# Kernel optimization log

Measured on AMD Instinct MI355X. Metric: run time of the kernel, lower is better.

Reference implementation:

```python
import jax, jax.numpy as jnp
import numpy as np


def setup_inputs() -> dict:
    key = jax.random.key(0)
    k1, k2, k3, k4 = jax.random.split(key, 4)
    N, E, d_i, d_o = 4096, 32768, 128, 128
    x = jax.random.normal(k1, (N, d_i), dtype=jnp.float32)
    src = jax.random.uniform(k2, (N, E), dtype=jnp.float32)
    tgt = jax.random.uniform(k3, (N, E), dtype=jnp.float32)
    # Linear(2*d_i, d_o): weight [d_o, 2*d_i] (xavier-like scale), bias zeros
    f_w = jax.random.normal(k4, (d_o, 2 * d_i), dtype=jnp.float32) * (1.0 / np.sqrt(2 * d_i))
    f_b = jnp.zeros((d_o,), dtype=jnp.float32)
    return {"x": x, "src": src, "tgt": tgt, "f_w": f_w, "f_b": f_b}


def reference(x, src, tgt, f_w, f_b):
    # gather node features to edges via dense incidence matmuls
    hsrc = src.T @ x                      # [E, d_i]
    htgt = tgt.T @ x                      # [E, d_i]
    h = jnp.concatenate([hsrc, htgt], axis=1)  # [E, 2*d_i]
    y = jax.nn.relu(h @ f_w.T + f_b)      # [E, d_o]
    return tgt @ y                        # scatter back to nodes: [N, d_o]
```

## Files before the change

kernel.cpp:

```cpp
#include <hip/hip_runtime.h>

typedef __attribute__((ext_vector_type(8))) short short8v;
typedef __attribute__((ext_vector_type(4))) float float4v;
typedef __attribute__((ext_vector_type(2))) unsigned int u32x2;
typedef __attribute__((ext_vector_type(4))) unsigned int u32x4;
typedef unsigned short u16;
typedef unsigned int u32;
typedef const __attribute__((address_space(1))) void* gas1;
typedef __attribute__((address_space(3))) void* las3;

#define NN 4096
#define EE 32768
#define DI 128
#define DO 128

__device__ __forceinline__ u16 f2bf(float f) {
    u32 u = __builtin_bit_cast(u32, f);
    u32 r = u + 0x7fffu + ((u >> 16) & 1u);
    return (u16)(r >> 16);
}
__device__ __forceinline__ u32 pack2bf(float lo, float hi) {
    return (u32)f2bf(lo) | ((u32)f2bf(hi) << 16);
}
__device__ __forceinline__ void gload16(const void* g, void* l) {
    __builtin_amdgcn_global_load_lds((gas1)g, (las3)l, 16, 0, 0);
}
__device__ __forceinline__ u32 cvtpk(float lo, float hi) {
    u32 r;
    asm("v_cvt_pk_bf16_f32 %0, %1, %2" : "=v"(r) : "v"(lo), "v"(hi));
    return r;
}

template<int R, int C>
__device__ __forceinline__ void stage_f32_bf16(char* lds, const float* src, int ld) {
    constexpr int CH = C / 8;
    constexpr int ITER = (R * CH) / 256;
#pragma unroll
    for (int it = 0; it < ITER; ++it) {
        int c = it * 256 + (int)threadIdx.x;
        int row = c / CH, col8 = c % CH;
        const float* p = src + (size_t)row * ld + col8 * 8;
        float4v v0 = *(const float4v*)p;
        float4v v1 = *(const float4v*)(p + 4);
        u32x4 w;
        w[0] = pack2bf(v0[0], v0[1]);
        w[1] = pack2bf(v0[2], v0[3]);
        w[2] = pack2bf(v1[0], v1[1]);
        w[3] = pack2bf(v1[2], v1[3]);
        int kb = col8 * 16;
        *(u32x4*)(lds + row * (C * 2) + (kb ^ ((row & 7) << 4))) = w;
    }
}
template<int ROWB>
__device__ __forceinline__ short8v ldfrag(const char* base, int row16, int kk) {
    int l = (int)threadIdx.x & 63;
    int row = row16 + (l & 15);
    int kb = kk * 64 + ((l >> 4) << 4);
    return *(const short8v*)(base + row * ROWB + (kb ^ ((row & 7) << 4)));
}

__global__ __launch_bounds__(256) void k1_ab(const float* __restrict__ x,
                                             const float* __restrict__ fw,
                                             u16* __restrict__ ATB) {
    __shared__ __align__(16) char lds[64 * 1024];
    char* aL = lds;
    char* bL = lds + 32 * 1024;
    int mb = (int)blockIdx.x >> 5, nb = (int)blockIdx.x & 31;
    stage_f32_bf16<128, 128>(aL, fw + mb * 128, 2 * DI);
    stage_f32_bf16<128, 128>(bL, x + (size_t)nb * 128 * DI, DI);
    __syncthreads();
    int w = (int)threadIdx.x >> 6, l = (int)threadIdx.x & 63;
    int wr = w >> 1, wc = w & 1;
    float4v acc[4][4] = {};
#pragma unroll
    for (int kk = 0; kk < 4; ++kk) {
        short8v af[4], bf[4];
#pragma unroll
        for (int m = 0; m < 4; ++m) af[m] = ldfrag<256>(aL, wr * 64 + m * 16, kk);
#pragma unroll
        for (int n2 = 0; n2 < 4; ++n2) bf[n2] = ldfrag<256>(bL, wc * 64 + n2 * 16, kk);
#pragma unroll
        for (int m = 0; m < 4; ++m)
#pragma unroll
            for (int n2 = 0; n2 < 4; ++n2)
                acc[m][n2] = __builtin_amdgcn_mfma_f32_16x16x32_bf16(af[m], bf[n2], acc[m][n2], 0, 0, 0);
    }
#pragma unroll
    for (int m = 0; m < 4; ++m)
#pragma unroll
        for (int n2 = 0; n2 < 4; ++n2)
#pragma unroll
            for (int r = 0; r < 4; ++r) {
                int mo = mb * 128 + wr * 64 + m * 16 + ((l >> 4) << 2) + r;
                int n  = nb * 128 + wc * 64 + n2 * 16 + (l & 15);
                ATB[(size_t)mo * NN + n] = f2bf(acc[m][n2][r]);
            }
}

__global__ __launch_bounds__(256, 2) void k2_y(const float* __restrict__ src,
                                               const float* __restrict__ tgt,
                                               const u16* __restrict__ ATB,
                                               const float* __restrict__ fb,
                                               u16* __restrict__ YT) {
    __shared__ __align__(16) char lds[48 * 1024];
    const int eb = (int)blockIdx.x * 64;
    const int t = (int)threadIdx.x, w = t >> 6, l = t & 63;
    const int eq = t & 15, nq = t >> 4;

    float4v r0, r1, r2, r3;
    auto loadT = [&](int ks) {
        const float* M = (ks >= 64 ? tgt : src);
        const int n0 = (ks & 63) * 64;
        const float* p = M + (size_t)(n0 + nq * 4) * EE + eb + eq * 4;
        r0 = *(const float4v*)p;
        r1 = *(const float4v*)(p + EE);
        r2 = *(const float4v*)(p + 2 * EE);
        r3 = *(const float4v*)(p + 3 * EE);
    };
    auto gloadA = [&](int ks, int p) {
        const int mat = ks >> 6, n0 = (ks & 63) * 64;
        const u16* AB = ATB + (size_t)mat * 128 * NN + n0;
#pragma unroll
        for (int q = 0; q < 4; ++q) {
            const int s = w * 4 + q;
            const int r = s * 8 + (l >> 3);
            const u16* ga = AB + (size_t)r * NN + (((l & 7) ^ (r & 7)) << 3);
            gload16(ga, lds + p * 16384 + s * 1024);
        }
    };
    auto writeT = [&](int p) {
        char* buf = lds + 32768 + p * 8192;
#pragma unroll
        for (int j = 0; j < 4; ++j) {
            int e = eq * 4 + j;
            u32x2 w2;
            w2[0] = cvtpk(r0[j], r1[j]);
            w2[1] = cvtpk(r2[j], r3[j]);
            *(u32x2*)(buf + e * 128 + ((nq * 8) ^ ((e & 7) << 4))) = w2;
        }
    };

    loadT(0);
    gloadA(0, 0);
    writeT(0);
    __syncthreads();

    float4v acc[2][4] = {};
    for (int ks = 0; ks < 128; ++ks) {
        const int nx = ks < 127 ? ks + 1 : 127;
        loadT(nx);
        gloadA(nx, (ks + 1) & 1);
        asm volatile("s_waitcnt vmcnt(8)" ::: "memory");
        __builtin_amdgcn_sched_barrier(0);
        const char* bufA = lds + (ks & 1) * 16384;
        const char* bufB = lds + 32768 + (ks & 1) * 8192;
        short8v af[2][2], bfr[2][4];
#pragma unroll
        for (int kk = 0; kk < 2; ++kk) {
#pragma unroll
            for (int m = 0; m < 2; ++m)
                af[kk][m] = ldfrag<128>(bufA, w * 32 + m * 16, kk);
#pragma unroll
            for (int n2 = 0; n2 < 4; ++n2)
                bfr[kk][n2] = ldfrag<128>(bufB, n2 * 16, kk);
        }
#pragma unroll
        for (int kk = 0; kk < 2; ++kk)
#pragma unroll
            for (int m = 0; m < 2; ++m)
#pragma unroll
                for (int n2 = 0; n2 < 4; ++n2)
                    acc[m][n2] = __builtin_amdgcn_mfma_f32_16x16x32_bf16(
                        af[kk][m], bfr[kk][n2], acc[m][n2], 0, 0, 0);
        asm volatile("s_waitcnt vmcnt(4)" ::: "memory");
        __builtin_amdgcn_sched_barrier(0);
        writeT((ks + 1) & 1);
        asm volatile("s_waitcnt lgkmcnt(0)" ::: "memory");
        __builtin_amdgcn_sched_barrier(0);
        __builtin_amdgcn_s_barrier();
    }
#pragma unroll
    for (int m = 0; m < 2; ++m)
#pragma unroll
        for (int n2 = 0; n2 < 4; ++n2)
#pragma unroll
            for (int r = 0; r < 4; ++r) {
                const int o = w * 32 + m * 16 + ((l >> 4) << 2) + r;
                const int e = eb + n2 * 16 + (l & 15);
                float v = acc[m][n2][r] + fb[o];
                v = v > 0.f ? v : 0.f;
                YT[(size_t)o * EE + e] = f2bf(v);
            }
}

__global__ __launch_bounds__(256, 2) void k3_part(const float* __restrict__ tgt,
                                                  const u16* __restrict__ YT,
                                                  float* __restrict__ part) {
    __shared__ __align__(16) char lds[64 * 1024];
    const int bid = (int)blockIdx.x;
    const int mb = bid & 63, kc = bid >> 6;
    const int e0 = kc * 2048;
    const int t = (int)threadIdx.x, w = t >> 6, l = t & 63;
    const int wr = w >> 1, wc = w & 1;

    auto stage = [&](int es, int p) {
        const int ec = e0 + es * 64;
#pragma unroll
        for (int q = 0; q < 4; ++q) {
            const int s = w * 4 + q;
            {
                const int r = s * 4 + (l >> 4);
                const float* gp = tgt + (size_t)(mb * 64 + r) * EE + ec
                                  + (((l & 15) ^ (r & 7)) << 2);
                gload16(gp, lds + p * 16384 + s * 1024);
            }
            {
                const int r = s * 8 + (l >> 3);
                const u16* gy = YT + (size_t)r * EE + ec + (((l & 7) ^ (r & 7)) << 3);
                gload16(gy, lds + 32768 + p * 16384 + s * 1024);
            }
        }
    };

    stage(0, 0);
    float4v acc[2][4] = {};
    for (int es = 0; es < 32; ++es) {
        stage(es < 31 ? es + 1 : 31, (es + 1) & 1);
        asm volatile("s_waitcnt vmcnt(8)" ::: "memory");
        __builtin_amdgcn_sched_barrier(0);
        __builtin_amdgcn_s_barrier();
        const char* bufT = lds + (es & 1) * 16384;
        const char* bufY = lds + 32768 + (es & 1) * 16384;
#pragma unroll
        for (int kk = 0; kk < 2; ++kk) {
            short8v af[2];
#pragma unroll
            for (int m = 0; m < 2; ++m) {
                const int row = wr * 32 + m * 16 + (l & 15);
                const int c0 = kk * 8 + ((l >> 4) << 1);
                float4v v0 = *(const float4v*)(bufT + row * 256 + ((c0 ^ (row & 7)) << 4));
                float4v v1 = *(const float4v*)(bufT + row * 256 + (((c0 + 1) ^ (row & 7)) << 4));
                u32x4 aw;
                aw[0] = cvtpk(v0[0], v0[1]);
                aw[1] = cvtpk(v0[2], v0[3]);
                aw[2] = cvtpk(v1[0], v1[1]);
                aw[3] = cvtpk(v1[2], v1[3]);
                af[m] = __builtin_bit_cast(short8v, aw);
            }
#pragma unroll
            for (int n2 = 0; n2 < 4; ++n2) {
                const int row = wc * 64 + n2 * 16 + (l & 15);
                short8v bf = *(const short8v*)(bufY + row * 128 +
                             ((kk * 64 + ((l >> 4) << 4)) ^ ((row & 7) << 4)));
#pragma unroll
                for (int m = 0; m < 2; ++m)
                    acc[m][n2] = __builtin_amdgcn_mfma_f32_16x16x32_bf16(
                        af[m], bf, acc[m][n2], 0, 0, 0);
            }
        }
        __builtin_amdgcn_sched_barrier(0);
        __builtin_amdgcn_s_barrier();
    }
#pragma unroll
    for (int m = 0; m < 2; ++m)
#pragma unroll
        for (int n2 = 0; n2 < 4; ++n2)
#pragma unroll
            for (int r = 0; r < 4; ++r) {
                const int n = mb * 64 + wr * 32 + m * 16 + ((l >> 4) << 2) + r;
                const int o = wc * 64 + n2 * 16 + (l & 15);
                part[((size_t)kc * NN + n) * DO + o] = acc[m][n2][r];
            }
}

__global__ __launch_bounds__(256) void k4_red(const float* __restrict__ part,
                                              float* __restrict__ out) {
    size_t i = ((size_t)blockIdx.x * 256 + threadIdx.x) * 4;
    float4v s = {0.f, 0.f, 0.f, 0.f};
#pragma unroll
    for (int kc = 0; kc < 16; ++kc)
        s += *(const float4v*)(part + (size_t)kc * NN * DO + i);
    *(float4v*)(out + i) = s;
}

extern "C" void kernel_launch(void* const* d_in, const int* in_sizes, int n_in,
                              void* d_out, int out_size, void* d_ws, size_t ws_size,
                              hipStream_t stream) {
    const float* x   = (const float*)d_in[0];
    const float* src = (const float*)d_in[1];
    const float* tgt = (const float*)d_in[2];
    const float* fw  = (const float*)d_in[3];
    const float* fb  = (const float*)d_in[4];
    float* out = (float*)d_out;

    char* ws = (char*)d_ws;
    u16*   ATB  = (u16*)ws;
    u16*   YT   = (u16*)(ws + (size_t)2 * 1024 * 1024);
    float* PART = (float*)(ws + (size_t)16 * 1024 * 1024);

    k1_ab  <<<64,   256, 0, stream>>>(x, fw, ATB);
    k2_y   <<<512,  256, 0, stream>>>(src, tgt, ATB, fb, YT);
    k3_part<<<1024, 256, 0, stream>>>(tgt, YT, PART);
    k4_red <<<512,  256, 0, stream>>>(PART, out);
}
```

Before: 320.1 us.

## Halve k2 edge tile for more blocks; stage tgt as bf16 in k3 LDS

k2_y now handles 32 edges per block instead of 64 and launches 1024 blocks. It uses less LDS and fewer accumulators, and its launch bound targets 4 blocks per SM, so the tgt/src streaming spreads across more CUs. k3_part now loads tgt through registers and converts it to bf16 once before writing to LDS. This replaces the old path that staged fp32 and converted during every fragment read, shrinking LDS so 3 blocks fit per SM. The trade-off is less data reuse per k2 block, since the ATB tile is now reloaded for every 32 edges, plus extra register-staged loads in k3.

```diff
diff --git a/kernel.cpp b/kernel.cpp
--- a/kernel.cpp
+++ b/kernel.cpp
@@ -97,25 +97,23 @@
             }
 }
 
-__global__ __launch_bounds__(256, 2) void k2_y(const float* __restrict__ src,
+__global__ __launch_bounds__(256, 4) void k2_y(const float* __restrict__ src,
                                                const float* __restrict__ tgt,
                                                const u16* __restrict__ ATB,
                                                const float* __restrict__ fb,
                                                u16* __restrict__ YT) {
-    __shared__ __align__(16) char lds[48 * 1024];
-    const int eb = (int)blockIdx.x * 64;
+    __shared__ __align__(16) char lds[40 * 1024];
+    const int eb = (int)blockIdx.x * 32;
     const int t = (int)threadIdx.x, w = t >> 6, l = t & 63;
-    const int eq = t & 15, nq = t >> 4;
-
-    float4v r0, r1, r2, r3;
+    const int eq = t & 7, np = t >> 3;
+
+    float4v r0, r1;
     auto loadT = [&](int ks) {
         const float* M = (ks >= 64 ? tgt : src);
         const int n0 = (ks & 63) * 64;
-        const float* p = M + (size_t)(n0 + nq * 4) * EE + eb + eq * 4;
+        const float* p = M + (size_t)(n0 + 2 * np) * EE + eb + eq * 4;
         r0 = *(const float4v*)p;
         r1 = *(const float4v*)(p + EE);
-        r2 = *(const float4v*)(p + 2 * EE);
-        r3 = *(const float4v*)(p + 3 * EE);
     };
     auto gloadA = [&](int ks, int p) {
         const int mat = ks >> 6, n0 = (ks & 63) * 64;
@@ -129,14 +127,11 @@
         }
     };
     auto writeT = [&](int p) {
-        char* buf = lds + 32768 + p * 8192;
+        char* buf = lds + 32768 + p * 4096;
 #pragma unroll
         for (int j = 0; j < 4; ++j) {
             int e = eq * 4 + j;
-            u32x2 w2;
-            w2[0] = cvtpk(r0[j], r1[j]);
-            w2[1] = cvtpk(r2[j], r3[j]);
-            *(u32x2*)(buf + e * 128 + ((nq * 8) ^ ((e & 7) << 4))) = w2;
+            *(u32*)(buf + e * 128 + ((np * 4) ^ ((e & 7) << 4))) = cvtpk(r0[j], r1[j]);
         }
     };
 
@@ -145,23 +140,23 @@
     writeT(0);
     __syncthreads();
 
-    float4v acc[2][4] = {};
+    float4v acc[2][2] = {};
     for (int ks = 0; ks < 128; ++ks) {
         const int nx = ks < 127 ? ks + 1 : 127;
         loadT(nx);
         gloadA(nx, (ks + 1) & 1);
-        asm volatile("s_waitcnt vmcnt(8)" ::: "memory");
+        asm volatile("s_waitcnt vmcnt(6)" ::: "memory");
         __builtin_amdgcn_sched_barrier(0);
         const char* bufA = lds + (ks & 1) * 16384;
-        const char* bufB = lds + 32768 + (ks & 1) * 8192;
-        short8v af[2][2], bfr[2][4];
+        const char* bufB = lds + 32768 + (ks & 1) * 4096;
+        short8v af[2][2], bfr[2][2];
 #pragma unroll
         for (int kk = 0; kk < 2; ++kk) {
 #pragma unroll
             for (int m = 0; m < 2; ++m)
                 af[kk][m] = ldfrag<128>(bufA, w * 32 + m * 16, kk);
 #pragma unroll
-            for (int n2 = 0; n2 < 4; ++n2)
+            for (int n2 = 0; n2 < 2; ++n2)
                 bfr[kk][n2] = ldfrag<128>(bufB, n2 * 16, kk);
         }
 #pragma unroll
@@ -169,7 +164,7 @@
 #pragma unroll
             for (int m = 0; m < 2; ++m)
 #pragma unroll
-                for (int n2 = 0; n2 < 4; ++n2)
+                for (int n2 = 0; n2 < 2; ++n2)
                     acc[m][n2] = __builtin_amdgcn_mfma_f32_16x16x32_bf16(
                         af[kk][m], bfr[kk][n2], acc[m][n2], 0, 0, 0);
         asm volatile("s_waitcnt vmcnt(4)" ::: "memory");
@@ -182,7 +177,7 @@
 #pragma unroll
     for (int m = 0; m < 2; ++m)
 #pragma unroll
-        for (int n2 = 0; n2 < 4; ++n2)
+        for (int n2 = 0; n2 < 2; ++n2)
 #pragma unroll
             for (int r = 0; r < 4; ++r) {
                 const int o = w * 32 + m * 16 + ((l >> 4) << 2) + r;
@@ -193,71 +188,83 @@
             }
 }
 
-__global__ __launch_bounds__(256, 2) void k3_part(const float* __restrict__ tgt,
+__global__ __launch_bounds__(256, 3) void k3_part(const float* __restrict__ tgt,
                                                   const u16* __restrict__ YT,
                                                   float* __restrict__ part) {
-    __shared__ __align__(16) char lds[64 * 1024];
+    __shared__ __align__(16) char lds[48 * 1024];
     const int bid = (int)blockIdx.x;
     const int mb = bid & 63, kc = bid >> 6;
     const int e0 = kc * 2048;
     const int t = (int)threadIdx.x, w = t >> 6, l = t & 63;
     const int wr = w >> 1, wc = w & 1;
-
-    auto stage = [&](int es, int p) {
+    const int trow = t >> 2, te0 = (t & 3) * 16;
+
+    float4v v0, v1, v2, v3;
+    auto loadT = [&](int es) {
+        const float* p = tgt + (size_t)(mb * 64 + trow) * EE + e0 + es * 64 + te0;
+        v0 = *(const float4v*)p;
+        v1 = *(const float4v*)(p + 4);
+        v2 = *(const float4v*)(p + 8);
+        v3 = *(const float4v*)(p + 12);
+    };
+    auto gloadY = [&](int es, int p) {
         const int ec = e0 + es * 64;
 #pragma unroll
         for (int q = 0; q < 4; ++q) {
             const int s = w * 4 + q;
-            {
-                const int r = s * 4 + (l >> 4);
-                const float* gp = tgt + (size_t)(mb * 64 + r) * EE + ec
-                                  + (((l & 15) ^ (r & 7)) << 2);
-                gload16(gp, lds + p * 16384 + s * 1024);
-            }
-            {
-                const int r = s * 8 + (l >> 3);
-                const u16* gy = YT + (size_t)r * EE + ec + (((l & 7) ^ (r & 7)) << 3);
-                gload16(gy, lds + 32768 + p * 16384 + s * 1024);
-            }
-        }
-    };
-
-    stage(0, 0);
+            const int r = s * 8 + (l >> 3);
+            const u16* gy = YT + (size_t)r * EE + ec + (((l & 7) ^ (r & 7)) << 3);
+            gload16(gy, lds + 16384 + p * 16384 + s * 1024);
+        }
+    };
+    auto writeT = [&](int p) {
+        char* buf = lds + p * 8192;
+        u32x4 wA, wB;
+        wA[0] = cvtpk(v0[0], v0[1]); wA[1] = cvtpk(v0[2], v0[3]);
+        wA[2] = cvtpk(v1[0], v1[1]); wA[3] = cvtpk(v1[2], v1[3]);
+        wB[0] = cvtpk(v2[0], v2[1]); wB[1] = cvtpk(v2[2], v2[3]);
+        wB[2] = cvtpk(v3[0], v3[1]); wB[3] = cvtpk(v3[2], v3[3]);
+        *(u32x4*)(buf + trow * 128 + ((te0 * 2) ^ ((trow & 7) << 4))) = wA;
+        *(u32x4*)(buf + trow * 128 + ((te0 * 2 + 16) ^ ((trow & 7) << 4))) = wB;
+    };
+
+    loadT(0);
+    gloadY(0, 0);
+    writeT(0);
+    __syncthreads();
+
     float4v acc[2][4] = {};
     for (int es = 0; es < 32; ++es) {
-        stage(es < 31 ? es + 1 : 31, (es + 1) & 1);
+        const int nx = es < 31 ? es + 1 : 31;
+        loadT(nx);
+        gloadY(nx, (es + 1) & 1);
         asm volatile("s_waitcnt vmcnt(8)" ::: "memory");
         __builtin_amdgcn_sched_barrier(0);
         __builtin_amdgcn_s_barrier();
-        const char* bufT = lds + (es & 1) * 16384;
-        const char* bufY = lds + 32768 + (es & 1) * 16384;
+        const char* bufT = lds + (es & 1) * 8192;
+        const char* bufY = lds + 16384 + (es & 1) * 16384;
+        short8v af[2][2], bfr[2][4];
 #pragma unroll
         for (int kk = 0; kk < 2; ++kk) {
-            short8v af[2];
-#pragma unroll
-            for (int m = 0; m < 2; ++m) {
-                const int row = wr * 32 + m * 16 + (l & 15);
-                const int c0 = kk * 8 + ((l >> 4) << 1);
-                float4v v0 = *(const float4v*)(bufT + row * 256 + ((c0 ^ (row & 7)) << 4));
-                float4v v1 = *(const float4v*)(bufT + row * 256 + (((c0 + 1) ^ (row & 7)) << 4));
-                u32x4 aw;
-                aw[0] = cvtpk(v0[0], v0[1]);
-                aw[1] = cvtpk(v0[2], v0[3]);
-                aw[2] = cvtpk(v1[0], v1[1]);
-                aw[3] = cvtpk(v1[2], v1[3]);
-                af[m] = __builtin_bit_cast(short8v, aw);
-            }
-#pragma unroll
-            for (int n2 = 0; n2 < 4; ++n2) {
-                const int row = wc * 64 + n2 * 16 + (l & 15);
-                short8v bf = *(const short8v*)(bufY + row * 128 +
-                             ((kk * 64 + ((l >> 4) << 4)) ^ ((row & 7) << 4)));
-#pragma unroll
-                for (int m = 0; m < 2; ++m)
+#pragma unroll
+            for (int m = 0; m < 2; ++m)
+                af[kk][m] = ldfrag<128>(bufT, wr * 32 + m * 16, kk);
+#pragma unroll
+            for (int n2 = 0; n2 < 4; ++n2)
+                bfr[kk][n2] = ldfrag<128>(bufY, wc * 64 + n2 * 16, kk);
+        }
+#pragma unroll
+        for (int kk = 0; kk < 2; ++kk)
+#pragma unroll
+            for (int m = 0; m < 2; ++m)
+#pragma unroll
+                for (int n2 = 0; n2 < 4; ++n2)
                     acc[m][n2] = __builtin_amdgcn_mfma_f32_16x16x32_bf16(
-                        af[m], bf, acc[m][n2], 0, 0, 0);
-            }
-        }
+                        af[kk][m], bfr[kk][n2], acc[m][n2], 0, 0, 0);
+        asm volatile("s_waitcnt vmcnt(4)" ::: "memory");
+        __builtin_amdgcn_sched_barrier(0);
+        writeT((es + 1) & 1);
+        asm volatile("s_waitcnt lgkmcnt(0)" ::: "memory");
         __builtin_amdgcn_sched_barrier(0);
         __builtin_amdgcn_s_barrier();
     }
@@ -299,7 +306,7 @@
     float* PART = (float*)(ws + (size_t)16 * 1024 * 1024);
 
     k1_ab  <<<64,   256, 0, stream>>>(x, fw, ATB);
-    k2_y   <<<512,  256, 0, stream>>>(src, tgt, ATB, fb, YT);
+    k2_y   <<<1024, 256, 0, stream>>>(src, tgt, ATB, fb, YT);
     k3_part<<<1024, 256, 0, stream>>>(tgt, YT, PART);
     k4_red <<<512,  256, 0, stream>>>(PART, out);
 }
```

Result: slower. 444.1 us (+38.7%).

## Split k2 node reduction in halves with fp32 partials and combine kernel

Applied to the files above, without the earlier changes.

The k2 GEMM is split along the node (K) dimension into two halves, doubling the grid from 512 to 1024 blocks so more CUs have work. Each block writes fp32 partial sums to a new workspace buffer. A new k2b_comb kernel adds the two partials and applies bias, ReLU and the bf16 conversion. The launch-bounds occupancy hint also rises from 2 to 3. The cost is an extra kernel launch and about 32 MB of extra fp32 write and read traffic.

```diff
diff --git a/kernel.cpp b/kernel.cpp
--- a/kernel.cpp
+++ b/kernel.cpp
@@ -97,20 +97,22 @@
             }
 }
 
-__global__ __launch_bounds__(256, 2) void k2_y(const float* __restrict__ src,
+__global__ __launch_bounds__(256, 3) void k2_y(const float* __restrict__ src,
                                                const float* __restrict__ tgt,
                                                const u16* __restrict__ ATB,
-                                               const float* __restrict__ fb,
-                                               u16* __restrict__ YT) {
+                                               float* __restrict__ PY) {
     __shared__ __align__(16) char lds[48 * 1024];
-    const int eb = (int)blockIdx.x * 64;
+    const int bid = (int)blockIdx.x;
+    const int eb = (bid >> 1) * 64;
+    const int nh = bid & 1;
+    const int nbase = nh * 2048;
     const int t = (int)threadIdx.x, w = t >> 6, l = t & 63;
     const int eq = t & 15, nq = t >> 4;
 
     float4v r0, r1, r2, r3;
     auto loadT = [&](int ks) {
-        const float* M = (ks >= 64 ? tgt : src);
-        const int n0 = (ks & 63) * 64;
+        const float* M = (ks >= 32 ? tgt : src);
+        const int n0 = nbase + (ks & 31) * 64;
         const float* p = M + (size_t)(n0 + nq * 4) * EE + eb + eq * 4;
         r0 = *(const float4v*)p;
         r1 = *(const float4v*)(p + EE);
@@ -118,7 +120,7 @@
         r3 = *(const float4v*)(p + 3 * EE);
     };
     auto gloadA = [&](int ks, int p) {
-        const int mat = ks >> 6, n0 = (ks & 63) * 64;
+        const int mat = ks >> 5, n0 = nbase + (ks & 31) * 64;
         const u16* AB = ATB + (size_t)mat * 128 * NN + n0;
 #pragma unroll
         for (int q = 0; q < 4; ++q) {
@@ -146,8 +148,8 @@
     __syncthreads();
 
     float4v acc[2][4] = {};
-    for (int ks = 0; ks < 128; ++ks) {
-        const int nx = ks < 127 ? ks + 1 : 127;
+    for (int ks = 0; ks < 64; ++ks) {
+        const int nx = ks < 63 ? ks + 1 : 63;
         loadT(nx);
         gloadA(nx, (ks + 1) & 1);
         asm volatile("s_waitcnt vmcnt(8)" ::: "memory");
@@ -179,6 +181,7 @@
         __builtin_amdgcn_sched_barrier(0);
         __builtin_amdgcn_s_barrier();
     }
+    float* PO = PY + (size_t)nh * 128 * EE;
 #pragma unroll
     for (int m = 0; m < 2; ++m)
 #pragma unroll
@@ -187,10 +190,27 @@
             for (int r = 0; r < 4; ++r) {
                 const int o = w * 32 + m * 16 + ((l >> 4) << 2) + r;
                 const int e = eb + n2 * 16 + (l & 15);
-                float v = acc[m][n2][r] + fb[o];
-                v = v > 0.f ? v : 0.f;
-                YT[(size_t)o * EE + e] = f2bf(v);
-            }
+                PO[(size_t)o * EE + e] = acc[m][n2][r];
+            }
+}
+
+__global__ __launch_bounds__(256) void k2b_comb(const float* __restrict__ PY,
+                                                const float* __restrict__ fb,
+                                                u16* __restrict__ YT) {
+    size_t f = ((size_t)blockIdx.x * 256 + threadIdx.x) * 4;
+    int o = (int)(f >> 15);
+    float4v s = *(const float4v*)(PY + f);
+    s += *(const float4v*)(PY + (size_t)128 * EE + f);
+    float b = fb[o];
+    float v0 = s[0] + b, v1 = s[1] + b, v2 = s[2] + b, v3 = s[3] + b;
+    v0 = v0 > 0.f ? v0 : 0.f;
+    v1 = v1 > 0.f ? v1 : 0.f;
+    v2 = v2 > 0.f ? v2 : 0.f;
+    v3 = v3 > 0.f ? v3 : 0.f;
+    u32x2 w2;
+    w2[0] = pack2bf(v0, v1);
+    w2[1] = pack2bf(v2, v3);
+    *(u32x2*)(YT + f) = w2;
 }
 
 __global__ __launch_bounds__(256, 2) void k3_part(const float* __restrict__ tgt,
@@ -296,10 +316,12 @@
     char* ws = (char*)d_ws;
     u16*   ATB  = (u16*)ws;
     u16*   YT   = (u16*)(ws + (size_t)2 * 1024 * 1024);
-    float* PART = (float*)(ws + (size_t)16 * 1024 * 1024);
-
-    k1_ab  <<<64,   256, 0, stream>>>(x, fw, ATB);
-    k2_y   <<<512,  256, 0, stream>>>(src, tgt, ATB, fb, YT);
-    k3_part<<<1024, 256, 0, stream>>>(tgt, YT, PART);
-    k4_red <<<512,  256, 0, stream>>>(PART, out);
-}
+    float* PY   = (float*)(ws + (size_t)16 * 1024 * 1024);
+    float* PART = (float*)(ws + (size_t)48 * 1024 * 1024);
+
+    k1_ab   <<<64,   256, 0, stream>>>(x, fw, ATB);
+    k2_y    <<<1024, 256, 0, stream>>>(src, tgt, ATB, PY);
+    k2b_comb<<<4096, 256, 0, stream>>>(PY, fb, YT);
+    k3_part <<<1024, 256, 0, stream>>>(tgt, YT, PART);
+    k4_red  <<<512,  256, 0, stream>>>(PART, out);
+}
```

Result: slower. 399.0 us (+24.6%).

## Load k2 A-fragments directly into registers, shrink LDS, raise occupancy

Applied to the files above, without the earlier changes.

In k2_y the A operand (ATB) is now read by each wave straight from global memory into registers in MFMA fragment layout. This replaces the async copy into a double-buffered LDS region. The A register buffers are ping-ponged by unrolling the k-loop by two, LDS drops to the T tile only, and launch bounds allow 3 blocks per SM. The aim is to cut LDS traffic and footprint and gain occupancy, at the cost of more VGPRs and less coalesced per-wave global loads. The waitcnt accounting (vmcnt(4)) now mixes A and T loads, which may be fragile.

```diff
diff --git a/kernel.cpp b/kernel.cpp
--- a/kernel.cpp
+++ b/kernel.cpp
@@ -97,12 +97,12 @@
             }
 }
 
-__global__ __launch_bounds__(256, 2) void k2_y(const float* __restrict__ src,
+__global__ __launch_bounds__(256, 3) void k2_y(const float* __restrict__ src,
                                                const float* __restrict__ tgt,
                                                const u16* __restrict__ ATB,
                                                const float* __restrict__ fb,
                                                u16* __restrict__ YT) {
-    __shared__ __align__(16) char lds[48 * 1024];
+    __shared__ __align__(16) char lds[16 * 1024];
     const int eb = (int)blockIdx.x * 64;
     const int t = (int)threadIdx.x, w = t >> 6, l = t & 63;
     const int eq = t & 15, nq = t >> 4;
@@ -117,19 +117,17 @@
         r2 = *(const float4v*)(p + 2 * EE);
         r3 = *(const float4v*)(p + 3 * EE);
     };
-    auto gloadA = [&](int ks, int p) {
+    auto loadA = [&](int ks, short8v& A00, short8v& A01, short8v& A10, short8v& A11) {
         const int mat = ks >> 6, n0 = (ks & 63) * 64;
-        const u16* AB = ATB + (size_t)mat * 128 * NN + n0;
-#pragma unroll
-        for (int q = 0; q < 4; ++q) {
-            const int s = w * 4 + q;
-            const int r = s * 8 + (l >> 3);
-            const u16* ga = AB + (size_t)r * NN + (((l & 7) ^ (r & 7)) << 3);
-            gload16(ga, lds + p * 16384 + s * 1024);
-        }
+        const u16* base = ATB + (size_t)(mat * 128 + w * 32 + (l & 15)) * NN
+                          + n0 + ((l >> 4) << 3);
+        A00 = *(const short8v*)(base);
+        A01 = *(const short8v*)(base + 32);
+        A10 = *(const short8v*)(base + (size_t)16 * NN);
+        A11 = *(const short8v*)(base + (size_t)16 * NN + 32);
     };
     auto writeT = [&](int p) {
-        char* buf = lds + 32768 + p * 8192;
+        char* buf = lds + p * 8192;
 #pragma unroll
         for (int j = 0; j < 4; ++j) {
             int e = eq * 4 + j;
@@ -140,44 +138,45 @@
         }
     };
 
+    short8v aA00, aA01, aA10, aA11, bA00, bA01, bA10, bA11;
     loadT(0);
-    gloadA(0, 0);
+    asm volatile("s_waitcnt vmcnt(0)" ::: "memory");
     writeT(0);
+    loadA(0, aA00, aA01, aA10, aA11);
     __syncthreads();
 
     float4v acc[2][4] = {};
-    for (int ks = 0; ks < 128; ++ks) {
+    auto step = [&](int ks,
+                    short8v& c00, short8v& c01, short8v& c10, short8v& c11,
+                    short8v& x00, short8v& x01, short8v& x10, short8v& x11) {
         const int nx = ks < 127 ? ks + 1 : 127;
         loadT(nx);
-        gloadA(nx, (ks + 1) & 1);
-        asm volatile("s_waitcnt vmcnt(8)" ::: "memory");
-        __builtin_amdgcn_sched_barrier(0);
-        const char* bufA = lds + (ks & 1) * 16384;
-        const char* bufB = lds + 32768 + (ks & 1) * 8192;
-        short8v af[2][2], bfr[2][4];
-#pragma unroll
-        for (int kk = 0; kk < 2; ++kk) {
-#pragma unroll
-            for (int m = 0; m < 2; ++m)
-                af[kk][m] = ldfrag<128>(bufA, w * 32 + m * 16, kk);
+        loadA(nx, x00, x01, x10, x11);
+        const char* bufB = lds + (ks & 1) * 8192;
+        short8v bfr[2][4];
+#pragma unroll
+        for (int kk = 0; kk < 2; ++kk)
 #pragma unroll
             for (int n2 = 0; n2 < 4; ++n2)
                 bfr[kk][n2] = ldfrag<128>(bufB, n2 * 16, kk);
+#pragma unroll
+        for (int n2 = 0; n2 < 4; ++n2) {
+            acc[0][n2] = __builtin_amdgcn_mfma_f32_16x16x32_bf16(c00, bfr[0][n2], acc[0][n2], 0, 0, 0);
+            acc[1][n2] = __builtin_amdgcn_mfma_f32_16x16x32_bf16(c10, bfr[0][n2], acc[1][n2], 0, 0, 0);
+            acc[0][n2] = __builtin_amdgcn_mfma_f32_16x16x32_bf16(c01, bfr[1][n2], acc[0][n2], 0, 0, 0);
+            acc[1][n2] = __builtin_amdgcn_mfma_f32_16x16x32_bf16(c11, bfr[1][n2], acc[1][n2], 0, 0, 0);
         }
-#pragma unroll
-        for (int kk = 0; kk < 2; ++kk)
-#pragma unroll
-            for (int m = 0; m < 2; ++m)
-#pragma unroll
-                for (int n2 = 0; n2 < 4; ++n2)
-                    acc[m][n2] = __builtin_amdgcn_mfma_f32_16x16x32_bf16(
-                        af[kk][m], bfr[kk][n2], acc[m][n2], 0, 0, 0);
         asm volatile("s_waitcnt vmcnt(4)" ::: "memory");
         __builtin_amdgcn_sched_barrier(0);
         writeT((ks + 1) & 1);
         asm volatile("s_waitcnt lgkmcnt(0)" ::: "memory");
         __builtin_amdgcn_sched_barrier(0);
         __builtin_amdgcn_s_barrier();
+    };
+
+    for (int ks = 0; ks < 128; ks += 2) {
+        step(ks,     aA00, aA01, aA10, aA11,  bA00, bA01, bA10, bA11);
+        step(ks + 1, bA00, bA01, bA10, bA11,  aA00, aA01, aA10, aA11);
     }
 #pragma unroll
     for (int m = 0; m < 2; ++m)
```

Measured after the change: 349.1 us. +9.1%, slower.
